# Kernel tuning notes

Measured on AMD Instinct MI355X. Metric: run time of the kernel, lower is better.

The kernel has to match this reference:

```python
import jax, jax.numpy as jnp
import numpy as np

B, S, D = 8, 1024, 256
H, DH = 8, 32  # num_heads, head_dim; H*DH == D


def setup_inputs() -> dict:
    key = jax.random.key(0)
    ks = jax.random.split(key, 10)
    s = 0.02
    return {
        "q": jax.random.normal(ks[0], (B, S, D), jnp.float32),
        "k": jax.random.normal(ks[1], (B, S, D), jnp.float32),
        "v": jax.random.normal(ks[2], (B, S, D), jnp.float32),
        "mask": jnp.zeros((B, 1, 1, S), jnp.float32),  # additive mask
        "bias": jax.random.normal(ks[3], (1, H, S, S), jnp.float32),  # pair bias
        "Wq": jax.random.normal(ks[4], (H * DH, D), jnp.float32) * s,
        "Wk": jax.random.normal(ks[5], (H * DH, D), jnp.float32) * s,
        "Wv": jax.random.normal(ks[6], (H * DH, D), jnp.float32) * s,
        "Wg": jnp.zeros((H * DH, D), jnp.float32),   # gating init: zeros weight
        "bg": jnp.ones((H * DH,), jnp.float32),      # gating init: ones bias
        "Wo": jax.random.normal(ks[7], (D, H * DH), jnp.float32) * s,
    }


def reference(q, k, v, mask, bias, Wq, Wk, Wv, Wg, bg, Wo):
    norm = DH ** -0.5
    g = jnp.einsum('bsd,ed->bse', q, Wg) + bg            # [B,S,H*DH]
    qh = (jnp.einsum('bsd,ed->bse', q, Wq) * norm).reshape(B, S, H, DH)
    kh = jnp.einsum('bsd,ed->bse', k, Wk).reshape(B, S, H, DH)
    vh = jnp.einsum('bsd,ed->bse', v, Wv).reshape(B, S, H, DH)
    # scores [B,H,Q,K] with additive mask and pair bias (unicore softmax_dropout)
    attn = jnp.einsum('bqhd,bkhd->bhqk', qh, kh) + mask + bias
    attn = jax.nn.softmax(attn, axis=-1)
    o = jnp.einsum('bhqk,bkhd->bqhd', attn, vh).reshape(B, S, H * DH)
    o = jax.nn.sigmoid(g) * o                            # gating
    return jnp.einsum('bse,de->bsd', o, Wo)              # output proj, NO bias in fwd
```

## Files before the change

kernel.cpp:

```cpp
#include <hip/hip_runtime.h>


typedef __attribute__((ext_vector_type(4))) float f32x4;
typedef __attribute__((ext_vector_type(8))) unsigned short u16x8;
typedef __attribute__((ext_vector_type(8))) __bf16 bf16x8;

#define BB 8
#define SS 1024
#define DD 256
#define HH 8
#define DHD 32

__device__ __forceinline__ unsigned short f2b(float f) {
  unsigned u = __builtin_bit_cast(unsigned, f);
  u += 0x7fffu + ((u >> 16) & 1u);
  return (unsigned short)(u >> 16);
}
__device__ __forceinline__ float b2f(unsigned short s) {
  unsigned u = ((unsigned)s) << 16;
  return __builtin_bit_cast(float, u);
}
__device__ __forceinline__ f32x4 mfma16(u16x8 a, u16x8 b, f32x4 c) {
  return __builtin_amdgcn_mfma_f32_16x16x32_bf16(
      __builtin_bit_cast(bf16x8, a), __builtin_bit_cast(bf16x8, b), c, 0, 0, 0);
}

__global__ __launch_bounds__(256) void proj_kernel(
    const float* __restrict__ q, const float* __restrict__ k,
    const float* __restrict__ v,
    const float* __restrict__ Wq, const float* __restrict__ Wg,
    const float* __restrict__ Wk, const float* __restrict__ Wv,
    const float* __restrict__ bg,
    unsigned short* __restrict__ qh, unsigned short* __restrict__ kh,
    unsigned short* __restrict__ vh, unsigned short* __restrict__ sig) {
  const int slot = blockIdx.z;
  const float* A = (slot <= 1) ? q : (slot == 2 ? k : v);
  const float* W = (slot == 0) ? Wq : (slot == 1 ? Wg : (slot == 2 ? Wk : Wv));
  const int row0 = blockIdx.x * 64, col0 = blockIdx.y * 64;
  const int tid = threadIdx.x;
  const int w = tid >> 6, lane = tid & 63, g = lane >> 4, c = lane & 15;
  const int sr = tid >> 2, sc = tid & 3;

  __shared__ alignas(16) unsigned short As[64 * 32];
  __shared__ alignas(16) unsigned short Ws[64 * 32];

  const f32x4 zero = {0.f, 0.f, 0.f, 0.f};
  f32x4 acc[4] = {zero, zero, zero, zero};

  for (int kk = 0; kk < 8; ++kk) {
    __syncthreads();
    {
      const float* ap = A + (size_t)(row0 + sr) * DD + kk * 32 + sc * 8;
      f32x4 f0 = *(const f32x4*)ap;
      f32x4 f1 = *(const f32x4*)(ap + 4);
      u16x8 a8;
#pragma unroll
      for (int j = 0; j < 4; ++j) { a8[j] = f2b(f0[j]); a8[j + 4] = f2b(f1[j]); }
      ((u16x8*)As)[sr * 4 + (sc ^ ((sr >> 1) & 3))] = a8;

      const float* wp = W + (size_t)(col0 + sr) * DD + kk * 32 + sc * 8;
      f32x4 w0 = *(const f32x4*)wp;
      f32x4 w1 = *(const f32x4*)(wp + 4);
      u16x8 w8;
#pragma unroll
      for (int j = 0; j < 4; ++j) { w8[j] = f2b(w0[j]); w8[j + 4] = f2b(w1[j]); }
      ((u16x8*)Ws)[sr * 4 + (sc ^ ((sr >> 1) & 3))] = w8;
    }
    __syncthreads();
    const int arow = 16 * w + c;
    u16x8 af = ((u16x8*)As)[arow * 4 + (g ^ ((arow >> 1) & 3))];
#pragma unroll
    for (int n = 0; n < 4; ++n) {
      const int brow = 16 * n + c;
      u16x8 wf = ((u16x8*)Ws)[brow * 4 + (g ^ ((brow >> 1) & 3))];
      acc[n] = mfma16(af, wf, acc[n]);
    }
  }

#pragma unroll
  for (int n = 0; n < 4; ++n) {
#pragma unroll
    for (int r = 0; r < 4; ++r) {
      const int row = row0 + 16 * w + 4 * g + r;
      const int col = col0 + 16 * n + c;
      const size_t idx = (size_t)row * DD + col;
      const float val = acc[n][r];
      if (slot == 0)      qh[idx] = f2b(val * 0.17677669529663687f);
      else if (slot == 1) sig[idx] = f2b(1.0f / (1.0f + __expf(-(val + bg[col]))));
      else if (slot == 2) kh[idx] = f2b(val);
      else                vh[idx] = f2b(val);
    }
  }
}

__global__ __launch_bounds__(256) void attn_kernel(
    const unsigned short* __restrict__ qh, const unsigned short* __restrict__ kh,
    const unsigned short* __restrict__ vh, const unsigned short* __restrict__ sig,
    const float* __restrict__ mask, const float* __restrict__ bias,
    unsigned short* __restrict__ og) {
  const int qt = blockIdx.x, h = blockIdx.y, b = blockIdx.z;
  const int tid = threadIdx.x;
  const int w = tid >> 6, lane = tid & 63, g = lane >> 4, c = lane & 15;
  const int sr = tid >> 2, sc = tid & 3;

  __shared__ alignas(16) unsigned short Ks[64 * 32];
  __shared__ alignas(16) unsigned short Vt[32 * 64];
  __shared__ alignas(16) unsigned short Ps[4][16 * 64];

  const int qrow = b * SS + qt * 64 + w * 16 + c;
  const u16x8 qf = *(const u16x8*)(qh + (size_t)qrow * DD + h * DHD + g * 8);

  const f32x4 zero = {0.f, 0.f, 0.f, 0.f};
  f32x4 acc[2] = {zero, zero};
  float m_r[4] = {-1e30f, -1e30f, -1e30f, -1e30f};
  float l_r[4] = {0.f, 0.f, 0.f, 0.f};

  const float* maskb = mask + b * SS;
  const float* biasb = bias + ((size_t)(h * SS + qt * 64 + w * 16)) * SS;

  for (int kt = 0; kt < 16; ++kt) {
    __syncthreads();
    {
      const unsigned short* kp =
          kh + (size_t)(b * SS + kt * 64 + sr) * DD + h * DHD + sc * 8;
      ((u16x8*)Ks)[sr * 4 + (sc ^ ((sr >> 1) & 3))] = *(const u16x8*)kp;

      const unsigned short* vp =
          vh + (size_t)(b * SS + kt * 64 + sr) * DD + h * DHD + sc * 8;
      u16x8 vv = *(const u16x8*)vp;
#pragma unroll
      for (int j = 0; j < 8; ++j) {
        const int dh = sc * 8 + j;
        Vt[dh * 64 + (((sr >> 3) ^ (dh & 7)) << 3) + (sr & 7)] = vv[j];
      }
    }
    __syncthreads();

    f32x4 sv[4];
#pragma unroll
    for (int t = 0; t < 4; ++t) {
      const int krow = 16 * t + c;
      u16x8 kf = ((u16x8*)Ks)[krow * 4 + (g ^ ((krow >> 1) & 3))];
      sv[t] = mfma16(qf, kf, zero);
    }
#pragma unroll
    for (int t = 0; t < 4; ++t) {
      const float mk = maskb[kt * 64 + 16 * t + c];
#pragma unroll
      for (int r = 0; r < 4; ++r)
        sv[t][r] += mk + biasb[(size_t)(4 * g + r) * SS + kt * 64 + 16 * t + c];
    }
#pragma unroll
    for (int r = 0; r < 4; ++r) {
      float mx = fmaxf(fmaxf(sv[0][r], sv[1][r]), fmaxf(sv[2][r], sv[3][r]));
#pragma unroll
      for (int off = 1; off < 16; off <<= 1) mx = fmaxf(mx, __shfl_xor(mx, off));
      const float mnew = fmaxf(m_r[r], mx);
      const float scale = __expf(m_r[r] - mnew);
      float ps = 0.f;
#pragma unroll
      for (int t = 0; t < 4; ++t) {
        const float p = __expf(sv[t][r] - mnew);
        sv[t][r] = p;
        ps += p;
      }
#pragma unroll
      for (int off = 1; off < 16; off <<= 1) ps += __shfl_xor(ps, off);
      l_r[r] = l_r[r] * scale + ps;
      m_r[r] = mnew;
      acc[0][r] *= scale;
      acc[1][r] *= scale;
    }
    unsigned short* P = Ps[w];
#pragma unroll
    for (int r = 0; r < 4; ++r) {
      const int qq = 4 * g + r;
#pragma unroll
      for (int t = 0; t < 4; ++t) {
        const int kv = 16 * t + c;
        P[qq * 64 + (((kv >> 3) ^ (qq & 7)) << 3) + (kv & 7)] = f2b(sv[t][r]);
      }
    }
    __syncthreads();
#pragma unroll
    for (int s2 = 0; s2 < 2; ++s2) {
      u16x8 pf = ((u16x8*)P)[c * 8 + ((4 * s2 + g) ^ (c & 7))];
#pragma unroll
      for (int dt = 0; dt < 2; ++dt) {
        const int vrow = 16 * dt + c;
        u16x8 vf = ((u16x8*)Vt)[vrow * 8 + ((4 * s2 + g) ^ (vrow & 7))];
        acc[dt] = mfma16(pf, vf, acc[dt]);
      }
    }
  }

#pragma unroll
  for (int r = 0; r < 4; ++r) {
    const float inv = 1.0f / l_r[r];
    const int row = b * SS + qt * 64 + w * 16 + 4 * g + r;
#pragma unroll
    for (int dt = 0; dt < 2; ++dt) {
      const int col = h * DHD + 16 * dt + c;
      const size_t idx = (size_t)row * DD + col;
      og[idx] = f2b(acc[dt][r] * inv * b2f(sig[idx]));
    }
  }
}

__global__ __launch_bounds__(256) void outproj_kernel(
    const unsigned short* __restrict__ og, const float* __restrict__ Wo,
    float* __restrict__ out) {
  const int row0 = blockIdx.x * 64, col0 = blockIdx.y * 64;
  const int tid = threadIdx.x;
  const int w = tid >> 6, lane = tid & 63, g = lane >> 4, c = lane & 15;
  const int sr = tid >> 2, sc = tid & 3;

  __shared__ alignas(16) unsigned short As[64 * 32];
  __shared__ alignas(16) unsigned short Ws[64 * 32];

  const f32x4 zero = {0.f, 0.f, 0.f, 0.f};
  f32x4 acc[4] = {zero, zero, zero, zero};

  for (int kk = 0; kk < 8; ++kk) {
    __syncthreads();
    {
      const unsigned short* ap = og + (size_t)(row0 + sr) * DD + kk * 32 + sc * 8;
      ((u16x8*)As)[sr * 4 + (sc ^ ((sr >> 1) & 3))] = *(const u16x8*)ap;

      const float* wp = Wo + (size_t)(col0 + sr) * DD + kk * 32 + sc * 8;
      f32x4 w0 = *(const f32x4*)wp;
      f32x4 w1 = *(const f32x4*)(wp + 4);
      u16x8 w8;
#pragma unroll
      for (int j = 0; j < 4; ++j) { w8[j] = f2b(w0[j]); w8[j + 4] = f2b(w1[j]); }
      ((u16x8*)Ws)[sr * 4 + (sc ^ ((sr >> 1) & 3))] = w8;
    }
    __syncthreads();
    const int arow = 16 * w + c;
    u16x8 af = ((u16x8*)As)[arow * 4 + (g ^ ((arow >> 1) & 3))];
#pragma unroll
    for (int n = 0; n < 4; ++n) {
      const int brow = 16 * n + c;
      u16x8 wf = ((u16x8*)Ws)[brow * 4 + (g ^ ((brow >> 1) & 3))];
      acc[n] = mfma16(af, wf, acc[n]);
    }
  }

#pragma unroll
  for (int n = 0; n < 4; ++n) {
#pragma unroll
    for (int r = 0; r < 4; ++r) {
      const int row = row0 + 16 * w + 4 * g + r;
      const int col = col0 + 16 * n + c;
      out[(size_t)row * DD + col] = acc[n][r];
    }
  }
}

extern "C" void kernel_launch(void* const* d_in, const int* in_sizes, int n_in,
                              void* d_out, int out_size, void* d_ws,
                              size_t ws_size, hipStream_t stream) {
  const float* q    = (const float*)d_in[0];
  const float* k    = (const float*)d_in[1];
  const float* v    = (const float*)d_in[2];
  const float* mask = (const float*)d_in[3];
  const float* bias = (const float*)d_in[4];
  const float* Wq   = (const float*)d_in[5];
  const float* Wk   = (const float*)d_in[6];
  const float* Wv   = (const float*)d_in[7];
  const float* Wg   = (const float*)d_in[8];
  const float* bg   = (const float*)d_in[9];
  const float* Wo   = (const float*)d_in[10];
  float* out = (float*)d_out;

  char* ws = (char*)d_ws;
  unsigned short* qh  = (unsigned short*)(ws);
  unsigned short* kh  = (unsigned short*)(ws + (4u << 20));
  unsigned short* vh  = (unsigned short*)(ws + (8u << 20));
  unsigned short* sig = (unsigned short*)(ws + (12u << 20));
  unsigned short* og  = (unsigned short*)(ws + (16u << 20));

  hipLaunchKernelGGL(proj_kernel, dim3(128, 4, 4), dim3(256), 0, stream,
                     q, k, v, Wq, Wg, Wk, Wv, bg, qh, kh, vh, sig);
  hipLaunchKernelGGL(attn_kernel, dim3(16, HH, BB), dim3(256), 0, stream,
                     qh, kh, vh, sig, mask, bias, og);
  hipLaunchKernelGGL(outproj_kernel, dim3(128, 4), dim3(256), 0, stream,
                     og, Wo, out);
}
```

Measured before the change: 87.63 us.

## Transpose V in projection and drop LDS staging from attention loop

The projection kernel now writes V already transposed per batch and head, so the attention kernel can read K and V fragments straight from global memory instead of staging them through shared memory behind block-wide barriers. The score MFMA operands are swapped so each lane holds one query row, which turns the bias and mask loads into vectorised float4 reads along the key dimension and cuts softmax reductions to two cross-lane shuffles. Manual bf16 rounding is replaced with native __bf16 conversions. The cost is that every wave re-reads K and V from global memory or cache with no sharing inside the block, and the P round-trip through LDS now relies on wave-private buffers without a barrier.

New measurement: 127.2 us. 45.1% more time.

```diff
diff --git a/kernel.cpp b/kernel.cpp
--- a/kernel.cpp
+++ b/kernel.cpp
@@ -3,7 +3,9 @@
 
 typedef __attribute__((ext_vector_type(4))) float f32x4;
 typedef __attribute__((ext_vector_type(8))) unsigned short u16x8;
+typedef __attribute__((ext_vector_type(4))) unsigned short u16x4;
 typedef __attribute__((ext_vector_type(8))) __bf16 bf16x8;
+typedef __attribute__((ext_vector_type(4))) __bf16 bf16x4;
 
 #define BB 8
 #define SS 1024
@@ -11,11 +13,6 @@
 #define HH 8
 #define DHD 32
 
-__device__ __forceinline__ unsigned short f2b(float f) {
-  unsigned u = __builtin_bit_cast(unsigned, f);
-  u += 0x7fffu + ((u >> 16) & 1u);
-  return (unsigned short)(u >> 16);
-}
 __device__ __forceinline__ float b2f(unsigned short s) {
   unsigned u = ((unsigned)s) << 16;
   return __builtin_bit_cast(float, u);
@@ -32,7 +29,7 @@
     const float* __restrict__ Wk, const float* __restrict__ Wv,
     const float* __restrict__ bg,
     unsigned short* __restrict__ qh, unsigned short* __restrict__ kh,
-    unsigned short* __restrict__ vh, unsigned short* __restrict__ sig) {
+    unsigned short* __restrict__ vhT, unsigned short* __restrict__ sig) {
   const int slot = blockIdx.z;
   const float* A = (slot <= 1) ? q : (slot == 2 ? k : v);
   const float* W = (slot == 0) ? Wq : (slot == 1 ? Wg : (slot == 2 ? Wk : Wv));
@@ -53,18 +50,18 @@
       const float* ap = A + (size_t)(row0 + sr) * DD + kk * 32 + sc * 8;
       f32x4 f0 = *(const f32x4*)ap;
       f32x4 f1 = *(const f32x4*)(ap + 4);
-      u16x8 a8;
-#pragma unroll
-      for (int j = 0; j < 4; ++j) { a8[j] = f2b(f0[j]); a8[j + 4] = f2b(f1[j]); }
-      ((u16x8*)As)[sr * 4 + (sc ^ ((sr >> 1) & 3))] = a8;
+      bf16x8 a8;
+#pragma unroll
+      for (int j = 0; j < 4; ++j) { a8[j] = (__bf16)f0[j]; a8[j + 4] = (__bf16)f1[j]; }
+      ((u16x8*)As)[sr * 4 + (sc ^ ((sr >> 1) & 3))] = __builtin_bit_cast(u16x8, a8);
 
       const float* wp = W + (size_t)(col0 + sr) * DD + kk * 32 + sc * 8;
       f32x4 w0 = *(const f32x4*)wp;
       f32x4 w1 = *(const f32x4*)(wp + 4);
-      u16x8 w8;
-#pragma unroll
-      for (int j = 0; j < 4; ++j) { w8[j] = f2b(w0[j]); w8[j + 4] = f2b(w1[j]); }
-      ((u16x8*)Ws)[sr * 4 + (sc ^ ((sr >> 1) & 3))] = w8;
+      bf16x8 w8;
+#pragma unroll
+      for (int j = 0; j < 4; ++j) { w8[j] = (__bf16)w0[j]; w8[j + 4] = (__bf16)w1[j]; }
+      ((u16x8*)Ws)[sr * 4 + (sc ^ ((sr >> 1) & 3))] = __builtin_bit_cast(u16x8, w8);
     }
     __syncthreads();
     const int arow = 16 * w + c;
@@ -77,133 +74,137 @@
     }
   }
 
-#pragma unroll
-  for (int n = 0; n < 4; ++n) {
-#pragma unroll
-    for (int r = 0; r < 4; ++r) {
-      const int row = row0 + 16 * w + 4 * g + r;
+  if (slot == 3) {
+    const int row_base = row0 + 16 * w + 4 * g;
+    const int bb = row_base >> 10;
+    const int s0 = row_base & 1023;
+#pragma unroll
+    for (int n = 0; n < 4; ++n) {
       const int col = col0 + 16 * n + c;
-      const size_t idx = (size_t)row * DD + col;
-      const float val = acc[n][r];
-      if (slot == 0)      qh[idx] = f2b(val * 0.17677669529663687f);
-      else if (slot == 1) sig[idx] = f2b(1.0f / (1.0f + __expf(-(val + bg[col]))));
-      else if (slot == 2) kh[idx] = f2b(val);
-      else                vh[idx] = f2b(val);
+      bf16x4 pv;
+#pragma unroll
+      for (int r = 0; r < 4; ++r) pv[r] = (__bf16)acc[n][r];
+      *(u16x4*)(vhT + (size_t)(bb * 256 + col) * SS + s0) =
+          __builtin_bit_cast(u16x4, pv);
+    }
+  } else {
+#pragma unroll
+    for (int n = 0; n < 4; ++n) {
+#pragma unroll
+      for (int r = 0; r < 4; ++r) {
+        const int row = row0 + 16 * w + 4 * g + r;
+        const int col = col0 + 16 * n + c;
+        const size_t idx = (size_t)row * DD + col;
+        const float val = acc[n][r];
+        if (slot == 0)
+          qh[idx] = __builtin_bit_cast(unsigned short,
+                        (__bf16)(val * 0.17677669529663687f));
+        else if (slot == 1)
+          sig[idx] = __builtin_bit_cast(unsigned short,
+                         (__bf16)(1.0f / (1.0f + __expf(-(val + bg[col])))));
+        else
+          kh[idx] = __builtin_bit_cast(unsigned short, (__bf16)val);
+      }
     }
   }
 }
 
 __global__ __launch_bounds__(256) void attn_kernel(
     const unsigned short* __restrict__ qh, const unsigned short* __restrict__ kh,
-    const unsigned short* __restrict__ vh, const unsigned short* __restrict__ sig,
+    const unsigned short* __restrict__ vhT, const unsigned short* __restrict__ sig,
     const float* __restrict__ mask, const float* __restrict__ bias,
     unsigned short* __restrict__ og) {
   const int qt = blockIdx.x, h = blockIdx.y, b = blockIdx.z;
   const int tid = threadIdx.x;
   const int w = tid >> 6, lane = tid & 63, g = lane >> 4, c = lane & 15;
-  const int sr = tid >> 2, sc = tid & 3;
-
-  __shared__ alignas(16) unsigned short Ks[64 * 32];
-  __shared__ alignas(16) unsigned short Vt[32 * 64];
+
   __shared__ alignas(16) unsigned short Ps[4][16 * 64];
-
-  const int qrow = b * SS + qt * 64 + w * 16 + c;
-  const u16x8 qf = *(const u16x8*)(qh + (size_t)qrow * DD + h * DHD + g * 8);
+  unsigned short* P = Ps[w];
+
+  const int q0 = qt * 64 + w * 16;
+  const u16x8 qf =
+      *(const u16x8*)(qh + (size_t)(b * SS + q0 + c) * DD + h * DHD + g * 8);
 
   const f32x4 zero = {0.f, 0.f, 0.f, 0.f};
   f32x4 acc[2] = {zero, zero};
-  float m_r[4] = {-1e30f, -1e30f, -1e30f, -1e30f};
-  float l_r[4] = {0.f, 0.f, 0.f, 0.f};
+  float m_r = -1e30f, l_r = 0.f;
 
   const float* maskb = mask + b * SS;
-  const float* biasb = bias + ((size_t)(h * SS + qt * 64 + w * 16)) * SS;
+  const float* biasb = bias + (size_t)(h * SS + q0 + c) * SS;
+  const unsigned short* kbase = kh + (size_t)(b * SS) * DD + h * DHD + g * 8;
+  const unsigned short* vbase =
+      vhT + (size_t)((b * HH + h) * DHD + c) * SS + g * 8;
 
   for (int kt = 0; kt < 16; ++kt) {
-    __syncthreads();
-    {
-      const unsigned short* kp =
-          kh + (size_t)(b * SS + kt * 64 + sr) * DD + h * DHD + sc * 8;
-      ((u16x8*)Ks)[sr * 4 + (sc ^ ((sr >> 1) & 3))] = *(const u16x8*)kp;
-
-      const unsigned short* vp =
-          vh + (size_t)(b * SS + kt * 64 + sr) * DD + h * DHD + sc * 8;
-      u16x8 vv = *(const u16x8*)vp;
-#pragma unroll
-      for (int j = 0; j < 8; ++j) {
-        const int dh = sc * 8 + j;
-        Vt[dh * 64 + (((sr >> 3) ^ (dh & 7)) << 3) + (sr & 7)] = vv[j];
-      }
-    }
-    __syncthreads();
-
+    const int kv0 = kt * 64;
     f32x4 sv[4];
 #pragma unroll
     for (int t = 0; t < 4; ++t) {
-      const int krow = 16 * t + c;
-      u16x8 kf = ((u16x8*)Ks)[krow * 4 + (g ^ ((krow >> 1) & 3))];
-      sv[t] = mfma16(qf, kf, zero);
+      u16x8 kf = *(const u16x8*)(kbase + (size_t)(kv0 + 16 * t + c) * DD);
+      sv[t] = mfma16(kf, qf, zero);
     }
 #pragma unroll
     for (int t = 0; t < 4; ++t) {
-      const float mk = maskb[kt * 64 + 16 * t + c];
-#pragma unroll
-      for (int r = 0; r < 4; ++r)
-        sv[t][r] += mk + biasb[(size_t)(4 * g + r) * SS + kt * 64 + 16 * t + c];
-    }
-#pragma unroll
-    for (int r = 0; r < 4; ++r) {
-      float mx = fmaxf(fmaxf(sv[0][r], sv[1][r]), fmaxf(sv[2][r], sv[3][r]));
-#pragma unroll
-      for (int off = 1; off < 16; off <<= 1) mx = fmaxf(mx, __shfl_xor(mx, off));
-      const float mnew = fmaxf(m_r[r], mx);
-      const float scale = __expf(m_r[r] - mnew);
-      float ps = 0.f;
-#pragma unroll
-      for (int t = 0; t < 4; ++t) {
+      const f32x4 bi = *(const f32x4*)(biasb + kv0 + 16 * t + 4 * g);
+      const f32x4 mk = *(const f32x4*)(maskb + kv0 + 16 * t + 4 * g);
+#pragma unroll
+      for (int r = 0; r < 4; ++r) sv[t][r] += mk[r] + bi[r];
+    }
+    float mx = fmaxf(fmaxf(sv[0][0], sv[0][1]), fmaxf(sv[0][2], sv[0][3]));
+#pragma unroll
+    for (int t = 1; t < 4; ++t)
+      mx = fmaxf(mx, fmaxf(fmaxf(sv[t][0], sv[t][1]), fmaxf(sv[t][2], sv[t][3])));
+    mx = fmaxf(mx, __shfl_xor(mx, 16));
+    mx = fmaxf(mx, __shfl_xor(mx, 32));
+    const float mnew = fmaxf(m_r, mx);
+    const float scale = __expf(m_r - mnew);
+    float ps = 0.f;
+#pragma unroll
+    for (int t = 0; t < 4; ++t)
+#pragma unroll
+      for (int r = 0; r < 4; ++r) {
         const float p = __expf(sv[t][r] - mnew);
         sv[t][r] = p;
         ps += p;
       }
-#pragma unroll
-      for (int off = 1; off < 16; off <<= 1) ps += __shfl_xor(ps, off);
-      l_r[r] = l_r[r] * scale + ps;
-      m_r[r] = mnew;
-      acc[0][r] *= scale;
-      acc[1][r] *= scale;
-    }
-    unsigned short* P = Ps[w];
-#pragma unroll
-    for (int r = 0; r < 4; ++r) {
-      const int qq = 4 * g + r;
-#pragma unroll
-      for (int t = 0; t < 4; ++t) {
-        const int kv = 16 * t + c;
-        P[qq * 64 + (((kv >> 3) ^ (qq & 7)) << 3) + (kv & 7)] = f2b(sv[t][r]);
+    ps += __shfl_xor(ps, 16);
+    ps += __shfl_xor(ps, 32);
+    l_r = l_r * scale + ps;
+    m_r = mnew;
+    acc[0] *= scale;
+    acc[1] *= scale;
+#pragma unroll
+    for (int t = 0; t < 4; ++t) {
+      bf16x4 pv;
+#pragma unroll
+      for (int r = 0; r < 4; ++r) pv[r] = (__bf16)sv[t][r];
+      const int n = 2 * t + (g >> 1);
+      *(u16x4*)(P + c * 64 + ((n ^ (c & 7)) << 3) + ((g & 1) << 2)) =
+          __builtin_bit_cast(u16x4, pv);
+    }
+#pragma unroll
+    for (int s2 = 0; s2 < 2; ++s2) {
+      const u16x8 pf =
+          *(const u16x8*)(P + c * 64 + (((4 * s2 + g) ^ (c & 7)) << 3));
+#pragma unroll
+      for (int dt = 0; dt < 2; ++dt) {
+        const u16x8 vf =
+            *(const u16x8*)(vbase + (size_t)(16 * dt) * SS + kv0 + 32 * s2);
+        acc[dt] = mfma16(vf, pf, acc[dt]);
       }
     }
-    __syncthreads();
-#pragma unroll
-    for (int s2 = 0; s2 < 2; ++s2) {
-      u16x8 pf = ((u16x8*)P)[c * 8 + ((4 * s2 + g) ^ (c & 7))];
-#pragma unroll
-      for (int dt = 0; dt < 2; ++dt) {
-        const int vrow = 16 * dt + c;
-        u16x8 vf = ((u16x8*)Vt)[vrow * 8 + ((4 * s2 + g) ^ (vrow & 7))];
-        acc[dt] = mfma16(pf, vf, acc[dt]);
-      }
-    }
-  }
-
-#pragma unroll
-  for (int r = 0; r < 4; ++r) {
-    const float inv = 1.0f / l_r[r];
-    const int row = b * SS + qt * 64 + w * 16 + 4 * g + r;
-#pragma unroll
-    for (int dt = 0; dt < 2; ++dt) {
-      const int col = h * DHD + 16 * dt + c;
-      const size_t idx = (size_t)row * DD + col;
-      og[idx] = f2b(acc[dt][r] * inv * b2f(sig[idx]));
-    }
+  }
+
+  const float inv = 1.0f / l_r;
+#pragma unroll
+  for (int dt = 0; dt < 2; ++dt) {
+    const size_t idx =
+        (size_t)(b * SS + q0 + c) * DD + h * DHD + 16 * dt + 4 * g;
+    const u16x4 sg = *(const u16x4*)(sig + idx);
+    bf16x4 ov;
+#pragma unroll
+    for (int r = 0; r < 4; ++r) ov[r] = (__bf16)(acc[dt][r] * inv * b2f(sg[r]));
+    *(u16x4*)(og + idx) = __builtin_bit_cast(u16x4, ov);
   }
 }
 
@@ -230,10 +231,10 @@
       const float* wp = Wo + (size_t)(col0 + sr) * DD + kk * 32 + sc * 8;
       f32x4 w0 = *(const f32x4*)wp;
       f32x4 w1 = *(const f32x4*)(wp + 4);
-      u16x8 w8;
-#pragma unroll
-      for (int j = 0; j < 4; ++j) { w8[j] = f2b(w0[j]); w8[j + 4] = f2b(w1[j]); }
-      ((u16x8*)Ws)[sr * 4 + (sc ^ ((sr >> 1) & 3))] = w8;
+      bf16x8 w8;
+#pragma unroll
+      for (int j = 0; j < 4; ++j) { w8[j] = (__bf16)w0[j]; w8[j + 4] = (__bf16)w1[j]; }
+      ((u16x8*)Ws)[sr * 4 + (sc ^ ((sr >> 1) & 3))] = __builtin_bit_cast(u16x8, w8);
     }
     __syncthreads();
     const int arow = 16 * w + c;
@@ -276,14 +277,14 @@
   char* ws = (char*)d_ws;
   unsigned short* qh  = (unsigned short*)(ws);
   unsigned short* kh  = (unsigned short*)(ws + (4u << 20));
-  unsigned short* vh  = (unsigned short*)(ws + (8u << 20));
+  unsigned short* vhT = (unsigned short*)(ws + (8u << 20));
   unsigned short* sig = (unsigned short*)(ws + (12u << 20));
   unsigned short* og  = (unsigned short*)(ws + (16u << 20));
 
   hipLaunchKernelGGL(proj_kernel, dim3(128, 4, 4), dim3(256), 0, stream,
-                     q, k, v, Wq, Wg, Wk, Wv, bg, qh, kh, vh, sig);
+                     q, k, v, Wq, Wg, Wk, Wv, bg, qh, kh, vhT, sig);
   hipLaunchKernelGGL(attn_kernel, dim3(16, HH, BB), dim3(256), 0, stream,
-                     qh, kh, vh, sig, mask, bias, og);
+                     qh, kh, vhT, sig, mask, bias, og);
   hipLaunchKernelGGL(outproj_kernel, dim3(128, 4), dim3(256), 0, stream,
                      og, Wo, out);
 }
```
